# Optimization experiments

Hardware: AMD Instinct MI355X
Metric: run time of the kernel (lower is better)

## Reference

```python
import jax, jax.numpy as jnp
import numpy as np

N_PROP = 1000
N_CLS = 81  # includes background class 0
IMG_H, IMG_W = 800, 1333
WX, WY, WW, WH = 10.0, 10.0, 5.0, 5.0
BBOX_XFORM_CLIP = float(np.log(1000.0 / 16.0))
SCORE_THRESH = 0.05
NMS_THRESH = 0.5
DET_PER_IMG = 100


def _decode(box_regression, proposals):
    widths = proposals[:, 2] - proposals[:, 0] + 1.0
    heights = proposals[:, 3] - proposals[:, 1] + 1.0
    ctr_x = proposals[:, 0] + 0.5 * widths
    ctr_y = proposals[:, 1] + 0.5 * heights
    rel = box_regression.reshape(box_regression.shape[0], -1, 4)  # [N, C, 4]
    dx = rel[..., 0] / WX
    dy = rel[..., 1] / WY
    dw = jnp.minimum(rel[..., 2] / WW, BBOX_XFORM_CLIP)
    dh = jnp.minimum(rel[..., 3] / WH, BBOX_XFORM_CLIP)
    pcx = dx * widths[:, None] + ctr_x[:, None]
    pcy = dy * heights[:, None] + ctr_y[:, None]
    pw = jnp.exp(dw) * widths[:, None]
    ph = jnp.exp(dh) * heights[:, None]
    return jnp.stack([pcx - 0.5 * pw, pcy - 0.5 * ph,
                      pcx + 0.5 * pw - 1.0, pcy + 0.5 * ph - 1.0], axis=-1)  # [N, C, 4]


def _clip_boxes(b, h, w):
    x1 = jnp.clip(b[..., 0], 0.0, w - 1.0)
    y1 = jnp.clip(b[..., 1], 0.0, h - 1.0)
    x2 = jnp.clip(b[..., 2], 0.0, w - 1.0)
    y2 = jnp.clip(b[..., 3], 0.0, h - 1.0)
    return jnp.stack([x1, y1, x2, y2], axis=-1)


def _nms_keep(boxes, scores, valid):
    # Greedy NMS for one class. boxes [N,4], scores [N], valid [N].
    # Returns keep mask in the ORIGINAL proposal order.
    n = scores.shape[0]
    order = jnp.argsort(-jnp.where(valid, scores, -jnp.inf))
    b = boxes[order]
    v = valid[order]
    x1, y1, x2, y2 = b[:, 0], b[:, 1], b[:, 2], b[:, 3]
    area = (x2 - x1 + 1.0) * (y2 - y1 + 1.0)
    iw = jnp.clip(jnp.minimum(x2[:, None], x2[None, :]) - jnp.maximum(x1[:, None], x1[None, :]) + 1.0, 0.0)
    ih = jnp.clip(jnp.minimum(y2[:, None], y2[None, :]) - jnp.maximum(y1[:, None], y1[None, :]) + 1.0, 0.0)
    inter = iw * ih
    iou = inter / (area[:, None] + area[None, :] - inter)
    idx = jnp.arange(n)

    def body(i, keep):
        sup = (iou[i] > NMS_THRESH) & (idx > i) & keep[i]
        return keep & ~sup

    keep = jax.lax.fori_loop(0, n, body, v)
    return jnp.zeros(n, dtype=bool).at[order].set(keep)


def _postprocess(class_logits, box_regression, proposal_boxes, image_h, image_w):
    prob = jax.nn.softmax(class_logits, axis=-1)             # [N, C]
    boxes = _decode(box_regression, proposal_boxes)           # [N, C, 4]
    boxes = _clip_boxes(boxes, float(image_h), float(image_w))
    scores_c = prob[:, 1:].T                                  # [C-1, N] skip background
    boxes_c = jnp.transpose(boxes[:, 1:, :], (1, 0, 2))       # [C-1, N, 4]
    valid = scores_c > SCORE_THRESH
    keep = jax.vmap(_nms_keep)(boxes_c, scores_c, valid)      # [C-1, N]
    masked = jnp.where(keep, scores_c, -jnp.inf)
    count = jnp.sum(keep)
    # torch.kthvalue(n - 100) == 101st largest kept score; keep scores >= it
    topv = jax.lax.top_k(masked.reshape(-1), DET_PER_IMG + 1)[0]
    image_thresh = jnp.where(count > DET_PER_IMG, topv[DET_PER_IMG], -jnp.inf)
    final = keep & (masked >= image_thresh)
    c1, n = scores_c.shape
    labels = jnp.broadcast_to(jnp.arange(1, c1 + 1, dtype=jnp.int32)[:, None], (c1, n))
    out_scores = jnp.where(final, scores_c, 0.0).reshape(-1)
    out_boxes = jnp.where(final[..., None], boxes_c, 0.0).reshape(-1, 4)
    out5 = jnp.concatenate([out_boxes, out_scores[:, None]], axis=1)  # [(C-1)*N, 5]
    return out5, jnp.where(final, labels, 0).reshape(-1), final.reshape(-1)


def setup_inputs() -> dict:
    key = jax.random.key(0)
    k1, k2, k3, k4 = jax.random.split(key, 4)
    # scale logits so a realistic fraction of softmax scores clears the 0.05 threshold
    class_logits = 3.0 * jax.random.normal(k1, (N_PROP, N_CLS), dtype=jnp.float32)
    box_regression = jax.random.normal(k2, (N_PROP, N_CLS * 4), dtype=jnp.float32)
    cxy = jax.random.uniform(k3, (N_PROP, 2), dtype=jnp.float32) * jnp.array([IMG_W, IMG_H], jnp.float32)
    wh = 16.0 + 284.0 * jax.random.uniform(k4, (N_PROP, 2), dtype=jnp.float32)
    x1y1 = jnp.clip(cxy - 0.5 * wh, 0.0)
    x2y2 = jnp.minimum(cxy + 0.5 * wh, jnp.array([IMG_W - 1.0, IMG_H - 1.0], jnp.float32))
    proposal_boxes = jnp.concatenate([x1y1, x2y2], axis=1)  # [N, 4] xyxy
    return {"class_logits": class_logits, "box_regression": box_regression,
            "proposal_boxes": proposal_boxes, "image_h": IMG_H, "image_w": IMG_W}


def reference(class_logits, box_regression, proposal_boxes, image_h, image_w):
    return _postprocess(class_logits, box_regression, proposal_boxes, image_h, image_w)
```

## Files before the change

### kernel.cpp

```cpp
#include <hip/hip_runtime.h>
#include <math.h>

#define N_PROP 1000
#define N_FG   80
#define SCORE_THRESH 0.05f
#define NMS_THRESH   0.5f
#define DET_PER_IMG  100
#define BBOX_CLIP    4.135166556742356f

#define LBL_OFF    400000
#define FIN_OFF    480000


__global__ __launch_bounds__(64)
void decode_softmax_kernel(const float* __restrict__ logits,
                           const float* __restrict__ reg,
                           const float* __restrict__ props,
                           const int* __restrict__ ih,
                           const int* __restrict__ iw,
                           float* __restrict__ out,
                           int* __restrict__ count) {
    const int n = blockIdx.x;
    const int t = threadIdx.x;
    if (n == 0 && t == 0) *count = 0;
    const float* lrow = logits + (size_t)n * 81;

    float v0 = lrow[t];
    float v1 = (t + 64 < 81) ? lrow[t + 64] : -INFINITY;
    float m = fmaxf(v0, v1);
    for (int off = 32; off; off >>= 1) m = fmaxf(m, __shfl_down(m, off));
    m = __shfl(m, 0);
    float e0 = expf(v0 - m);
    float e1 = (t + 64 < 81) ? expf(v1 - m) : 0.0f;
    float s = e0 + e1;
    for (int off = 32; off; off >>= 1) s += __shfl_down(s, off);
    s = __shfl(s, 0);

    const float px1 = props[n * 4 + 0];
    const float py1 = props[n * 4 + 1];
    const float px2 = props[n * 4 + 2];
    const float py2 = props[n * 4 + 3];
    const float w  = px2 - px1 + 1.0f;
    const float h  = py2 - py1 + 1.0f;
    const float cx = px1 + 0.5f * w;
    const float cy = py1 + 0.5f * h;
    const float W1 = (float)iw[0] - 1.0f;
    const float H1 = (float)ih[0] - 1.0f;

    #pragma unroll
    for (int k = 0; k < 2; ++k) {
        int cls = t + 1 + k * 64;
        if (cls <= 80) {
            const float* r = reg + ((size_t)n * 81 + cls) * 4;
            float dx = r[0] / 10.0f;
            float dy = r[1] / 10.0f;
            float dw = fminf(r[2] / 5.0f, BBOX_CLIP);
            float dh = fminf(r[3] / 5.0f, BBOX_CLIP);
            float pcx = dx * w + cx;
            float pcy = dy * h + cy;
            float pw = expf(dw) * w;
            float ph = expf(dh) * h;
            float bx1 = pcx - 0.5f * pw;
            float by1 = pcy - 0.5f * ph;
            float bx2 = pcx + 0.5f * pw - 1.0f;
            float by2 = pcy + 0.5f * ph - 1.0f;
            bx1 = fminf(fmaxf(bx1, 0.0f), W1);
            bx2 = fminf(fmaxf(bx2, 0.0f), W1);
            by1 = fminf(fmaxf(by1, 0.0f), H1);
            by2 = fminf(fmaxf(by2, 0.0f), H1);
            float p = expf(lrow[cls] - m) / s;
            size_t o = ((size_t)(cls - 1) * N_PROP + n) * 5;
            out[o + 0] = bx1;
            out[o + 1] = by1;
            out[o + 2] = bx2;
            out[o + 3] = by2;
            out[o + 4] = p;
        }
    }
}

__global__ __launch_bounds__(64)
void nms_kernel(const float* __restrict__ out5,
                unsigned char* __restrict__ keepFlags,
                float* __restrict__ compact,
                int* __restrict__ count) {
    const int c = blockIdx.x;
    const int lane = threadIdx.x;

    __shared__ float vssc[N_PROP];
    __shared__ int   vsidx[N_PROP];
    __shared__ int   spos[N_PROP];
    __shared__ float sx1[N_PROP], sy1[N_PROP], sx2[N_PROP], sy2[N_PROP];
    __shared__ float sar[N_PROP], ssc2[N_PROP];
    __shared__ int   sjdx[N_PROP];
    __shared__ unsigned char skeep[N_PROP];

    const float* base = out5 + (size_t)c * N_PROP * 5;

    int V = 0;
    #pragma unroll
    for (int it = 0; it < 16; ++it) {
        int j = it * 64 + lane;
        float sc = -1.0f;
        bool val = false;
        if (j < N_PROP) {
            sc = base[(size_t)j * 5 + 4];
            val = sc > SCORE_THRESH;
        }
        unsigned long long mask = __ballot(val);
        int pre = __popcll(mask & ((1ULL << lane) - 1ULL));
        if (val) { vssc[V + pre] = sc; vsidx[V + pre] = j; }
        V += __popcll(mask);
    }
    __syncthreads();

    for (int v = lane; v < V; v += 64) {
        float s = vssc[v];
        int id = vsidx[v];
        int r = 0;
        for (int u = 0; u < V; ++u) {
            float su = vssc[u];
            r += (su > s) || (su == s && vsidx[u] < id);
        }
        spos[v] = r;
    }
    __syncthreads();

    for (int v = lane; v < V; v += 64) {
        int r = spos[v];
        int j = vsidx[v];
        const float* bp = base + (size_t)j * 5;
        float x1 = bp[0], y1 = bp[1], x2 = bp[2], y2 = bp[3];
        sx1[r] = x1; sy1[r] = y1; sx2[r] = x2; sy2[r] = y2;
        sar[r] = (x2 - x1 + 1.0f) * (y2 - y1 + 1.0f);
        ssc2[r] = vssc[v];
        sjdx[r] = j;
        skeep[r] = 1;
    }
    __syncthreads();

    for (int r = 0; r < V; ++r) {
        bool alive = skeep[r] != 0;
        if (alive) {
            const float X1 = sx1[r], Y1 = sy1[r], X2 = sx2[r], Y2 = sy2[r], A = sar[r];
            for (int v = r + 1 + lane; v < V; v += 64) {
                if (skeep[v]) {
                    float iw = fminf(X2, sx2[v]) - fmaxf(X1, sx1[v]) + 1.0f;
                    float ihh = fminf(Y2, sy2[v]) - fmaxf(Y1, sy1[v]) + 1.0f;
                    iw = fmaxf(iw, 0.0f);
                    ihh = fmaxf(ihh, 0.0f);
                    float inter = iw * ihh;
                    float iou = inter / (A + sar[v] - inter);
                    if (iou > NMS_THRESH) skeep[v] = 0;
                }
            }
        }
        __syncthreads();
    }

    for (int j = lane; j < N_PROP; j += 64) keepFlags[c * N_PROP + j] = 0;
    __syncthreads();
    for (int r = lane; r < V; r += 64) {
        if (skeep[r]) {
            keepFlags[c * N_PROP + sjdx[r]] = 1;
            int pos = atomicAdd(count, 1);
            compact[pos] = ssc2[r];
        }
    }
}

__global__ __launch_bounds__(64)
void thresh_kernel(const float* __restrict__ compact,
                   const int* __restrict__ count,
                   float* __restrict__ thresh) {
    __shared__ float ls[8192];
    const int n = *count;
    const int lane = threadIdx.x;
    if (n <= DET_PER_IMG) {
        if (lane == 0) *thresh = 0.0f;
        return;
    }
    const bool useL = (n <= 8192);
    if (useL) {
        for (int i = lane; i < n; i += 64) ls[i] = compact[i];
    }
    __syncthreads();
    unsigned lo = 0u, hi = 0x40000000u;
    while (hi - lo > 1u) {
        unsigned mid = lo + ((hi - lo) >> 1);
        float mv = __uint_as_float(mid);
        int cnt = 0;
        if (useL) {
            for (int i = lane; i < n; i += 64) cnt += (ls[i] >= mv) ? 1 : 0;
        } else {
            for (int i = lane; i < n; i += 64) cnt += (compact[i] >= mv) ? 1 : 0;
        }
        for (int off = 32; off; off >>= 1) cnt += __shfl_down(cnt, off);
        cnt = __shfl(cnt, 0);
        if (cnt >= DET_PER_IMG + 1) lo = mid; else hi = mid;
    }
    if (lane == 0) *thresh = __uint_as_float(lo);
}

__global__ __launch_bounds__(256)
void finalize_kernel(float* __restrict__ out,
                     const unsigned char* __restrict__ keepFlags,
                     const float* __restrict__ thresh) {
    int idx = blockIdx.x * 256 + threadIdx.x;
    if (idx >= N_FG * N_PROP) return;
    const float th = *thresh;
    float sc = out[(size_t)idx * 5 + 4];
    bool fin = keepFlags[idx] && (sc >= th);
    if (!fin) {
        out[(size_t)idx * 5 + 0] = 0.0f;
        out[(size_t)idx * 5 + 1] = 0.0f;
        out[(size_t)idx * 5 + 2] = 0.0f;
        out[(size_t)idx * 5 + 3] = 0.0f;
        out[(size_t)idx * 5 + 4] = 0.0f;
    }
    int c = idx / N_PROP;
    out[LBL_OFF + idx] = fin ? (float)(c + 1) : 0.0f;
    out[FIN_OFF + idx] = fin ? 1.0f : 0.0f;
}

extern "C" void kernel_launch(void* const* d_in, const int* in_sizes, int n_in,
                              void* d_out, int out_size, void* d_ws, size_t ws_size,
                              hipStream_t stream) {
    const float* logits = (const float*)d_in[0];
    const float* reg    = (const float*)d_in[1];
    const float* props  = (const float*)d_in[2];
    const int*   ih     = (const int*)d_in[3];
    const int*   iw     = (const int*)d_in[4];
    float* out = (float*)d_out;

    char* ws = (char*)d_ws;
    int*   count   = (int*)(ws + 0);
    float* thresh  = (float*)(ws + 4);
    unsigned char* keepFlags = (unsigned char*)(ws + 16);
    float* compact = (float*)(ws + 80016);

    decode_softmax_kernel<<<N_PROP, 64, 0, stream>>>(logits, reg, props, ih, iw, out, count);
    nms_kernel<<<N_FG, 64, 0, stream>>>(out, keepFlags, compact, count);
    thresh_kernel<<<1, 64, 0, stream>>>(compact, count, thresh);
    finalize_kernel<<<(N_FG * N_PROP + 255) / 256, 256, 0, stream>>>(out, keepFlags, thresh);
}
```

Measured before the change: 80.32 us.

## Fuse decode, NMS, threshold and finalize into one cooperative kernel

Replaces the four separate launches with one cooperative kernel that uses grid-wide syncs between phases. Softmax probabilities go to a transposed workspace, and boxes are decoded only for proposals that pass the score threshold, inside each class's NMS block. Every NMS block recomputes the top-100 threshold on its own, and finalize writes only the kept rows over an output that was zeroed up front. This removes the inter-kernel gaps and the full-size decode writes, at the cost of two grid syncs and a redundant threshold search in each block.

```diff
diff --git a/kernel.cpp b/kernel.cpp
--- a/kernel.cpp
+++ b/kernel.cpp
@@ -1,7 +1,11 @@
 #include <hip/hip_runtime.h>
+#include <hip/hip_cooperative_groups.h>
 #include <math.h>
 
+namespace cg = cooperative_groups;
+
 #define N_PROP 1000
+#define N_CLS  81
 #define N_FG   80
 #define SCORE_THRESH 0.05f
 #define NMS_THRESH   0.5f
@@ -11,51 +15,109 @@
 #define LBL_OFF    400000
 #define FIN_OFF    480000
 
-
-__global__ __launch_bounds__(64)
-void decode_softmax_kernel(const float* __restrict__ logits,
-                           const float* __restrict__ reg,
-                           const float* __restrict__ props,
-                           const int* __restrict__ ih,
-                           const int* __restrict__ iw,
-                           float* __restrict__ out,
-                           int* __restrict__ count) {
-    const int n = blockIdx.x;
+#define NBLOCKS 160
+
+
+__global__ __launch_bounds__(256)
+void fused_kernel(const float* __restrict__ logits,
+                  const float* __restrict__ reg,
+                  const float* __restrict__ props,
+                  const int* __restrict__ ihp,
+                  const int* __restrict__ iwp,
+                  float* __restrict__ out,
+                  int* __restrict__ count,
+                  float* __restrict__ probT,
+                  float* __restrict__ compact)
+{
+    cg::grid_group grid = cg::this_grid();
+    const int b = blockIdx.x;
     const int t = threadIdx.x;
-    if (n == 0 && t == 0) *count = 0;
-    const float* lrow = logits + (size_t)n * 81;
-
-    float v0 = lrow[t];
-    float v1 = (t + 64 < 81) ? lrow[t + 64] : -INFINITY;
-    float m = fmaxf(v0, v1);
-    for (int off = 32; off; off >>= 1) m = fmaxf(m, __shfl_down(m, off));
-    m = __shfl(m, 0);
-    float e0 = expf(v0 - m);
-    float e1 = (t + 64 < 81) ? expf(v1 - m) : 0.0f;
-    float s = e0 + e1;
-    for (int off = 32; off; off >>= 1) s += __shfl_down(s, off);
-    s = __shfl(s, 0);
-
-    const float px1 = props[n * 4 + 0];
-    const float py1 = props[n * 4 + 1];
-    const float px2 = props[n * 4 + 2];
-    const float py2 = props[n * 4 + 3];
-    const float w  = px2 - px1 + 1.0f;
-    const float h  = py2 - py1 + 1.0f;
-    const float cx = px1 + 0.5f * w;
-    const float cy = py1 + 0.5f * h;
-    const float W1 = (float)iw[0] - 1.0f;
-    const float H1 = (float)ih[0] - 1.0f;
-
-    #pragma unroll
-    for (int k = 0; k < 2; ++k) {
-        int cls = t + 1 + k * 64;
-        if (cls <= 80) {
-            const float* r = reg + ((size_t)n * 81 + cls) * 4;
-            float dx = r[0] / 10.0f;
-            float dy = r[1] / 10.0f;
-            float dw = fminf(r[2] / 5.0f, BBOX_CLIP);
-            float dh = fminf(r[3] / 5.0f, BBOX_CLIP);
+    const int lane = t & 63;
+    const int wave = t >> 6;
+
+    __shared__ float sSc[N_PROP];
+    __shared__ int   sIdx[N_PROP];
+    __shared__ int   sPos[N_PROP];
+    __shared__ float sx1[N_PROP], sy1[N_PROP], sx2[N_PROP], sy2[N_PROP];
+    __shared__ float sar[N_PROP], sSc2[N_PROP];
+    __shared__ int   sJdx[N_PROP];
+    __shared__ unsigned char sKeep[N_PROP];
+    __shared__ int   shV;
+    __shared__ int   red4[4];
+    __shared__ float lsc[8192];
+
+    if (b == 0 && t == 0) *count = 0;
+    {
+        float4 z = make_float4(0.f, 0.f, 0.f, 0.f);
+        float4* o4 = (float4*)out;
+        for (int i = b * 256 + t; i < 140000; i += NBLOCKS * 256) o4[i] = z;
+    }
+    for (int n = b * 4 + wave; n < N_PROP; n += NBLOCKS * 4) {
+        const float* lrow = logits + (size_t)n * N_CLS;
+        float v0 = lrow[lane];
+        float v1 = (lane + 64 < N_CLS) ? lrow[lane + 64] : -INFINITY;
+        float m = fmaxf(v0, v1);
+        for (int off = 32; off; off >>= 1) m = fmaxf(m, __shfl_down(m, off));
+        m = __shfl(m, 0);
+        float e0 = expf(v0 - m);
+        float e1 = (lane + 64 < N_CLS) ? expf(v1 - m) : 0.0f;
+        float s = e0 + e1;
+        for (int off = 32; off; off >>= 1) s += __shfl_down(s, off);
+        s = __shfl(s, 0);
+        if (lane >= 1)           probT[(size_t)(lane - 1) * N_PROP + n] = e0 / s;
+        if (lane + 64 < N_CLS)   probT[(size_t)(lane + 63) * N_PROP + n] = e1 / s;
+    }
+    grid.sync();
+
+    if (b < N_FG) {
+        const int c = b;
+        for (int j = t; j < N_PROP; j += 256) sSc[j] = probT[(size_t)c * N_PROP + j];
+        __syncthreads();
+
+        if (wave == 0) {
+            int V = 0;
+            #pragma unroll
+            for (int it = 0; it < 16; ++it) {
+                int j = it * 64 + lane;
+                float sc = (j < N_PROP) ? sSc[j] : -1.0f;
+                bool val = (j < N_PROP) && (sc > SCORE_THRESH);
+                unsigned long long mask = __ballot(val);
+                int pre = __popcll(mask & ((1ULL << lane) - 1ULL));
+                if (val) { sSc[V + pre] = sc; sIdx[V + pre] = j; }
+                V += __popcll(mask);
+            }
+            if (lane == 0) shV = V;
+        }
+        __syncthreads();
+        const int V = shV;
+
+        for (int v = t; v < V; v += 256) {
+            float s = sSc[v];
+            int id = sIdx[v];
+            int r = 0;
+            for (int u = 0; u < V; ++u) {
+                float su = sSc[u];
+                r += (su > s) || (su == s && sIdx[u] < id);
+            }
+            sPos[v] = r;
+        }
+        __syncthreads();
+
+        const float W1 = (float)iwp[0] - 1.0f;
+        const float H1 = (float)ihp[0] - 1.0f;
+        for (int v = t; v < V; v += 256) {
+            int r = sPos[v];
+            int j = sIdx[v];
+            float4 pr = *(const float4*)(props + (size_t)j * 4);
+            float w  = pr.z - pr.x + 1.0f;
+            float h  = pr.w - pr.y + 1.0f;
+            float cx = pr.x + 0.5f * w;
+            float cy = pr.y + 0.5f * h;
+            float4 rr = *(const float4*)(reg + ((size_t)j * N_CLS + (c + 1)) * 4);
+            float dx = rr.x / 10.0f;
+            float dy = rr.y / 10.0f;
+            float dw = fminf(rr.z / 5.0f, BBOX_CLIP);
+            float dh = fminf(rr.w / 5.0f, BBOX_CLIP);
             float pcx = dx * w + cx;
             float pcy = dy * h + cy;
             float pw = expf(dw) * w;
@@ -68,159 +130,80 @@
             bx2 = fminf(fmaxf(bx2, 0.0f), W1);
             by1 = fminf(fmaxf(by1, 0.0f), H1);
             by2 = fminf(fmaxf(by2, 0.0f), H1);
-            float p = expf(lrow[cls] - m) / s;
-            size_t o = ((size_t)(cls - 1) * N_PROP + n) * 5;
-            out[o + 0] = bx1;
-            out[o + 1] = by1;
-            out[o + 2] = bx2;
-            out[o + 3] = by2;
-            out[o + 4] = p;
-        }
-    }
-}
-
-__global__ __launch_bounds__(64)
-void nms_kernel(const float* __restrict__ out5,
-                unsigned char* __restrict__ keepFlags,
-                float* __restrict__ compact,
-                int* __restrict__ count) {
-    const int c = blockIdx.x;
-    const int lane = threadIdx.x;
-
-    __shared__ float vssc[N_PROP];
-    __shared__ int   vsidx[N_PROP];
-    __shared__ int   spos[N_PROP];
-    __shared__ float sx1[N_PROP], sy1[N_PROP], sx2[N_PROP], sy2[N_PROP];
-    __shared__ float sar[N_PROP], ssc2[N_PROP];
-    __shared__ int   sjdx[N_PROP];
-    __shared__ unsigned char skeep[N_PROP];
-
-    const float* base = out5 + (size_t)c * N_PROP * 5;
-
-    int V = 0;
-    #pragma unroll
-    for (int it = 0; it < 16; ++it) {
-        int j = it * 64 + lane;
-        float sc = -1.0f;
-        bool val = false;
-        if (j < N_PROP) {
-            sc = base[(size_t)j * 5 + 4];
-            val = sc > SCORE_THRESH;
-        }
-        unsigned long long mask = __ballot(val);
-        int pre = __popcll(mask & ((1ULL << lane) - 1ULL));
-        if (val) { vssc[V + pre] = sc; vsidx[V + pre] = j; }
-        V += __popcll(mask);
-    }
-    __syncthreads();
-
-    for (int v = lane; v < V; v += 64) {
-        float s = vssc[v];
-        int id = vsidx[v];
-        int r = 0;
-        for (int u = 0; u < V; ++u) {
-            float su = vssc[u];
-            r += (su > s) || (su == s && vsidx[u] < id);
-        }
-        spos[v] = r;
-    }
-    __syncthreads();
-
-    for (int v = lane; v < V; v += 64) {
-        int r = spos[v];
-        int j = vsidx[v];
-        const float* bp = base + (size_t)j * 5;
-        float x1 = bp[0], y1 = bp[1], x2 = bp[2], y2 = bp[3];
-        sx1[r] = x1; sy1[r] = y1; sx2[r] = x2; sy2[r] = y2;
-        sar[r] = (x2 - x1 + 1.0f) * (y2 - y1 + 1.0f);
-        ssc2[r] = vssc[v];
-        sjdx[r] = j;
-        skeep[r] = 1;
-    }
-    __syncthreads();
-
-    for (int r = 0; r < V; ++r) {
-        bool alive = skeep[r] != 0;
-        if (alive) {
-            const float X1 = sx1[r], Y1 = sy1[r], X2 = sx2[r], Y2 = sy2[r], A = sar[r];
-            for (int v = r + 1 + lane; v < V; v += 64) {
-                if (skeep[v]) {
-                    float iw = fminf(X2, sx2[v]) - fmaxf(X1, sx1[v]) + 1.0f;
-                    float ihh = fminf(Y2, sy2[v]) - fmaxf(Y1, sy1[v]) + 1.0f;
-                    iw = fmaxf(iw, 0.0f);
-                    ihh = fmaxf(ihh, 0.0f);
-                    float inter = iw * ihh;
-                    float iou = inter / (A + sar[v] - inter);
-                    if (iou > NMS_THRESH) skeep[v] = 0;
+            sx1[r] = bx1; sy1[r] = by1; sx2[r] = bx2; sy2[r] = by2;
+            sar[r] = (bx2 - bx1 + 1.0f) * (by2 - by1 + 1.0f);
+            sSc2[r] = sSc[v];
+            sJdx[r] = j;
+            sKeep[r] = 1;
+        }
+        __syncthreads();
+
+        for (int r = 0; r < V; ++r) {
+            if (sKeep[r]) {
+                const float X1 = sx1[r], Y1 = sy1[r], X2 = sx2[r], Y2 = sy2[r], A = sar[r];
+                for (int v = r + 1 + t; v < V; v += 256) {
+                    if (sKeep[v]) {
+                        float iw = fminf(X2, sx2[v]) - fmaxf(X1, sx1[v]) + 1.0f;
+                        float ih = fminf(Y2, sy2[v]) - fmaxf(Y1, sy1[v]) + 1.0f;
+                        iw = fmaxf(iw, 0.0f);
+                        ih = fmaxf(ih, 0.0f);
+                        float inter = iw * ih;
+                        float iou = inter / (A + sar[v] - inter);
+                        if (iou > NMS_THRESH) sKeep[v] = 0;
+                    }
                 }
             }
-        }
-        __syncthreads();
-    }
-
-    for (int j = lane; j < N_PROP; j += 64) keepFlags[c * N_PROP + j] = 0;
-    __syncthreads();
-    for (int r = lane; r < V; r += 64) {
-        if (skeep[r]) {
-            keepFlags[c * N_PROP + sjdx[r]] = 1;
-            int pos = atomicAdd(count, 1);
-            compact[pos] = ssc2[r];
-        }
-    }
-}
-
-__global__ __launch_bounds__(64)
-void thresh_kernel(const float* __restrict__ compact,
-                   const int* __restrict__ count,
-                   float* __restrict__ thresh) {
-    __shared__ float ls[8192];
-    const int n = *count;
-    const int lane = threadIdx.x;
-    if (n <= DET_PER_IMG) {
-        if (lane == 0) *thresh = 0.0f;
-        return;
-    }
-    const bool useL = (n <= 8192);
-    if (useL) {
-        for (int i = lane; i < n; i += 64) ls[i] = compact[i];
-    }
-    __syncthreads();
-    unsigned lo = 0u, hi = 0x40000000u;
-    while (hi - lo > 1u) {
-        unsigned mid = lo + ((hi - lo) >> 1);
-        float mv = __uint_as_float(mid);
-        int cnt = 0;
-        if (useL) {
-            for (int i = lane; i < n; i += 64) cnt += (ls[i] >= mv) ? 1 : 0;
-        } else {
-            for (int i = lane; i < n; i += 64) cnt += (compact[i] >= mv) ? 1 : 0;
-        }
-        for (int off = 32; off; off >>= 1) cnt += __shfl_down(cnt, off);
-        cnt = __shfl(cnt, 0);
-        if (cnt >= DET_PER_IMG + 1) lo = mid; else hi = mid;
-    }
-    if (lane == 0) *thresh = __uint_as_float(lo);
-}
-
-__global__ __launch_bounds__(256)
-void finalize_kernel(float* __restrict__ out,
-                     const unsigned char* __restrict__ keepFlags,
-                     const float* __restrict__ thresh) {
-    int idx = blockIdx.x * 256 + threadIdx.x;
-    if (idx >= N_FG * N_PROP) return;
-    const float th = *thresh;
-    float sc = out[(size_t)idx * 5 + 4];
-    bool fin = keepFlags[idx] && (sc >= th);
-    if (!fin) {
-        out[(size_t)idx * 5 + 0] = 0.0f;
-        out[(size_t)idx * 5 + 1] = 0.0f;
-        out[(size_t)idx * 5 + 2] = 0.0f;
-        out[(size_t)idx * 5 + 3] = 0.0f;
-        out[(size_t)idx * 5 + 4] = 0.0f;
-    }
-    int c = idx / N_PROP;
-    out[LBL_OFF + idx] = fin ? (float)(c + 1) : 0.0f;
-    out[FIN_OFF + idx] = fin ? 1.0f : 0.0f;
+            __syncthreads();
+        }
+
+        for (int v = t; v < V; v += 256) {
+            if (sKeep[v]) {
+                int pos = atomicAdd(count, 1);
+                compact[pos] = sSc2[v];
+            }
+        }
+    }
+    grid.sync();
+
+    if (b < N_FG) {
+        const int n = *count;
+        float th = 0.0f;
+        if (n > DET_PER_IMG) {
+            const bool useL = (n <= 8192);
+            if (useL) {
+                for (int i = t; i < n; i += 256) lsc[i] = compact[i];
+                __syncthreads();
+            }
+            unsigned lo = 0u, hi = 0x40000000u;
+            while (hi - lo > 1u) {
+                unsigned mid = lo + ((hi - lo) >> 1);
+                float mv = __uint_as_float(mid);
+                int cnt = 0;
+                if (useL) { for (int i = t; i < n; i += 256) cnt += (lsc[i] >= mv) ? 1 : 0; }
+                else      { for (int i = t; i < n; i += 256) cnt += (compact[i] >= mv) ? 1 : 0; }
+                for (int off = 32; off; off >>= 1) cnt += __shfl_down(cnt, off);
+                if (lane == 0) red4[wave] = cnt;
+                __syncthreads();
+                int total = red4[0] + red4[1] + red4[2] + red4[3];
+                __syncthreads();
+                if (total >= DET_PER_IMG + 1) lo = mid; else hi = mid;
+            }
+            th = __uint_as_float(lo);
+        }
+        const int V = shV;
+        for (int r = t; r < V; r += 256) {
+            if (sKeep[r] && sSc2[r] >= th) {
+                size_t row = (size_t)b * N_PROP + sJdx[r];
+                out[row * 5 + 0] = sx1[r];
+                out[row * 5 + 1] = sy1[r];
+                out[row * 5 + 2] = sx2[r];
+                out[row * 5 + 3] = sy2[r];
+                out[row * 5 + 4] = sSc2[r];
+                out[LBL_OFF + row] = (float)(b + 1);
+                out[FIN_OFF + row] = 1.0f;
+            }
+        }
+    }
 }
 
 extern "C" void kernel_launch(void* const* d_in, const int* in_sizes, int n_in,
@@ -229,18 +212,16 @@
     const float* logits = (const float*)d_in[0];
     const float* reg    = (const float*)d_in[1];
     const float* props  = (const float*)d_in[2];
-    const int*   ih     = (const int*)d_in[3];
-    const int*   iw     = (const int*)d_in[4];
+    const int*   ihp    = (const int*)d_in[3];
+    const int*   iwp    = (const int*)d_in[4];
     float* out = (float*)d_out;
 
     char* ws = (char*)d_ws;
     int*   count   = (int*)(ws + 0);
-    float* thresh  = (float*)(ws + 4);
-    unsigned char* keepFlags = (unsigned char*)(ws + 16);
-    float* compact = (float*)(ws + 80016);
-
-    decode_softmax_kernel<<<N_PROP, 64, 0, stream>>>(logits, reg, props, ih, iw, out, count);
-    nms_kernel<<<N_FG, 64, 0, stream>>>(out, keepFlags, compact, count);
-    thresh_kernel<<<1, 64, 0, stream>>>(compact, count, thresh);
-    finalize_kernel<<<(N_FG * N_PROP + 255) / 256, 256, 0, stream>>>(out, keepFlags, thresh);
+    float* probT   = (float*)(ws + 64);
+    float* compact = (float*)(ws + 320064);
+
+    void* args[] = { (void*)&logits, (void*)&reg, (void*)&props, (void*)&ihp, (void*)&iwp,
+                     (void*)&out, (void*)&count, (void*)&probT, (void*)&compact };
+    hipLaunchCooperativeKernel((void*)fused_kernel, dim3(NBLOCKS), dim3(256), args, 0, stream);
 }
```

New measurement: 110.6 us. 1.38x slower.
